# Kernel tuning notes

Measured on AMD Instinct MI355X. Metric: run time of the kernel, lower is better.

The kernel has to match this reference:

```python
import jax, jax.numpy as jnp
import numpy as np

DIM = 1024
HID = 2048
E = 4

def setup_inputs() -> dict:
    key = jax.random.key(0)
    ks = jax.random.split(key, 7)
    s = lambda fan_in: 1.0 / np.sqrt(fan_in)
    x = jax.random.normal(ks[0], (2, 2048, DIM), dtype=jnp.float32)
    W1 = jax.random.uniform(ks[1], (E, DIM, HID), jnp.float32, -s(DIM), s(DIM))
    b1 = jax.random.uniform(ks[2], (E, HID), jnp.float32, -s(DIM), s(DIM))
    W2 = jax.random.uniform(ks[3], (E, HID, DIM), jnp.float32, -s(HID), s(HID))
    b2 = jax.random.uniform(ks[4], (E, DIM), jnp.float32, -s(HID), s(HID))
    Wr = jax.random.uniform(ks[5], (DIM, E), jnp.float32, -s(DIM), s(DIM))
    br = jax.random.uniform(ks[6], (E,), jnp.float32, -s(DIM), s(DIM))
    return {"x": x, "W1": W1, "b1": b1, "W2": W2, "b2": b2, "Wr": Wr, "br": br}

def reference(x, W1, b1, W2, b2, Wr, br):
    # router softmax weights: [B,T,E]
    weights = jax.nn.softmax(x @ Wr + br, axis=-1)
    # all-expert MLP: hidden [B,T,E,H]
    h = jax.nn.gelu(jnp.einsum('btd,edh->bteh', x, W1) + b1, approximate=False)
    # expert outputs [B,T,E,D]
    y = jnp.einsum('bteh,ehd->bted', h, W2) + b2
    # softmax-weighted combine over experts
    return jnp.einsum('bte,bted->btd', weights, y)
```

## Files before the change

### kernel.cpp

```cpp
#include <hip/hip_runtime.h>
#include <hip/hip_bf16.h>
#include <math.h>

#define DIM 1024
#define HID 2048
#define NE  4
#define NT  4096
#define KW  (NE*HID)
#define KSPLIT 2
#define KCH (KW / KSPLIT)

typedef __attribute__((ext_vector_type(8))) short short8;
typedef __attribute__((ext_vector_type(4))) short short4v;
typedef __attribute__((ext_vector_type(4))) float floatx4;


__device__ __forceinline__ void async_cp16(const void* g, void* l) {
  __builtin_amdgcn_global_load_lds(
      (const __attribute__((address_space(1))) void*)g,
      (__attribute__((address_space(3))) void*)l, 16, 0, 0);
}

__device__ __forceinline__ short f2bf(float f) {
  union { float f; unsigned u; } x; x.f = f;
  unsigned r = x.u + 0x7fffu + ((x.u >> 16) & 1u);
  return (short)(r >> 16);
}

__device__ __forceinline__ float gelu_fast(float v) {
  float u = 1.595769122f * (v + 0.044715f * v * v * v);
  return v * __builtin_amdgcn_rcpf(1.0f + __expf(-u));
}

#define WBAR(N) do { \
    asm volatile("s_waitcnt vmcnt(" #N ")" ::: "memory"); \
    __builtin_amdgcn_s_barrier(); \
  } while (0)

__global__ void router_cvt(const float* __restrict__ x, const float* __restrict__ Wr,
                           const float* __restrict__ br, float* __restrict__ wgt,
                           short* __restrict__ xb) {
  const int wv = threadIdx.x >> 6, lane = threadIdx.x & 63;
  const int t = blockIdx.x * 4 + wv;
  const float* xr = x + (size_t)t * DIM;
  short* xo = xb + (size_t)t * DIM;
  float a0 = 0.f, a1 = 0.f, a2 = 0.f, a3 = 0.f;
  #pragma unroll
  for (int p = 0; p < 4; p++) {
    const int d = p * 256 + lane * 4;
    floatx4 v = *(const floatx4*)&xr[d];
    short4v o;
    #pragma unroll
    for (int j = 0; j < 4; j++) {
      o[j] = f2bf(v[j]);
      floatx4 wr = *(const floatx4*)&Wr[(d + j) * 4];
      a0 += v[j] * wr[0]; a1 += v[j] * wr[1];
      a2 += v[j] * wr[2]; a3 += v[j] * wr[3];
    }
    *(short4v*)&xo[d] = o;
  }
  #pragma unroll
  for (int off = 32; off; off >>= 1) {
    a0 += __shfl_down(a0, off);
    a1 += __shfl_down(a1, off);
    a2 += __shfl_down(a2, off);
    a3 += __shfl_down(a3, off);
  }
  a0 = __shfl(a0, 0); a1 = __shfl(a1, 0); a2 = __shfl(a2, 0); a3 = __shfl(a3, 0);
  float s0 = a0 + br[0], s1 = a1 + br[1], s2 = a2 + br[2], s3 = a3 + br[3];
  float m = fmaxf(fmaxf(s0, s1), fmaxf(s2, s3));
  float e0 = __expf(s0 - m), e1 = __expf(s1 - m), e2 = __expf(s2 - m), e3 = __expf(s3 - m);
  float inv = 1.f / (e0 + e1 + e2 + e3);
  float v = (lane == 0) ? e0 : (lane == 1) ? e1 : (lane == 2) ? e2 : e3;
  if (lane < 4) wgt[t * 4 + lane] = v * inv;
}

#define TP_PADR 136
__global__ void transpose_all(const float* __restrict__ W1, short* __restrict__ w1t,
                              const float* __restrict__ W2, short* __restrict__ w2t) {
  __shared__ __align__(16) short tile[32 * TP_PADR];
  const int b = blockIdx.x;
  const float* in; short* out; int R, C, xt, yt;
  if (b < 2048) {
    const int e = b >> 9, rem = b & 511;
    xt = rem & 63; yt = rem >> 6; R = DIM; C = HID;
    in = W1 + (size_t)e * DIM * HID; out = w1t + (size_t)e * DIM * HID;
  } else {
    const int rem = b - 2048;
    xt = rem & 31; yt = rem >> 5; R = KW; C = DIM;
    in = W2; out = w2t;
  }
  const int c0 = xt * 32, r0 = yt * 128;
  const int t = threadIdx.x;
  const int cin = (t & 7) * 4;
  const int rin = t >> 3;
  #pragma unroll
  for (int i = 0; i < 4; i++) {
    const int r = rin + i * 32;
    floatx4 v = *(const floatx4*)&in[(size_t)(r0 + r) * C + c0 + cin];
    #pragma unroll
    for (int j = 0; j < 4; j++)
      tile[(cin + j) * TP_PADR + r] = f2bf(v[j]);
  }
  __syncthreads();
  const int ct = t >> 3;
  #pragma unroll
  for (int i = 0; i < 2; i++) {
    const int rc = (t & 7) + 8 * i;
    short8 vv = *(const short8*)&tile[ct * TP_PADR + rc * 8];
    *(short8*)&out[(size_t)(c0 + ct) * R + r0 + rc * 8] = vv;
  }
}


__global__ __launch_bounds__(512, 2)
void gemm1_kernel(const short* __restrict__ xb, const short* __restrict__ w1t,
                  const float* __restrict__ b1, const float* __restrict__ wgt,
                  short* __restrict__ hw) {
  __shared__ __align__(16) short lds[65536];
  const int b = blockIdx.x;
  const int xcd = b & 7, slot = b >> 3;
  const int m0 = ((xcd & 3) * 4 + (slot & 3)) * 256;
  const int n0 = ((xcd >> 2) * 16 + (slot >> 2)) * 256;
  const int tid = threadIdx.x;
  const int lane = tid & 63, wv = tid >> 6;
  const int wm = (wv >> 2) * 128, wn = (wv & 3) * 64;
  const int quad = lane >> 4, lrow = lane & 15;

  const int srow = tid >> 3, su = (tid & 7) ^ (srow & 7);
  const int sm = 2 * srow + (su >> 2), skc = su & 3;
  const short* srcA0 = xb + (size_t)(m0 + sm) * DIM + skc * 8;
  const short* srcA1 = srcA0 + (size_t)128 * DIM;
  const short* srcB0 = w1t + (size_t)(n0 + sm) * DIM + skc * 8;
  const short* srcB1 = srcB0 + (size_t)128 * DIM;

  const int cswz = (quad | ((lrow & 1) << 2)) ^ (lrow >> 1);
  const int offA = ((wm >> 1) + (lrow >> 1)) * 64 + cswz * 8;
  const int offB = ((wn >> 1) + (lrow >> 1)) * 64 + cswz * 8;

  floatx4 acc[8][4];
  #pragma unroll
  for (int i = 0; i < 8; i++)
    #pragma unroll
    for (int j = 0; j < 4; j++) acc[i][j] = (floatx4)0.f;

#define G1_STAGE(sl, tk) do { \
    short* Ab = &lds[(sl) * 8192]; short* Bb = &lds[32768 + (sl) * 8192]; \
    async_cp16(srcA0 + (tk) * 32, Ab + tid * 8); \
    async_cp16(srcA1 + (tk) * 32, Ab + 4096 + tid * 8); \
    async_cp16(srcB0 + (tk) * 32, Bb + tid * 8); \
    async_cp16(srcB1 + (tk) * 32, Bb + 4096 + tid * 8); \
  } while (0)

#define G1_COMP(sl) do { \
    const short* Ab = &lds[(sl) * 8192]; const short* Bb = &lds[32768 + (sl) * 8192]; \
    short8 af[8], bfr[4]; \
    _Pragma("unroll") for (int i = 0; i < 8; i++) \
      af[i] = *(const short8*)&Ab[offA + i * 512]; \
    _Pragma("unroll") for (int j = 0; j < 4; j++) \
      bfr[j] = *(const short8*)&Bb[offB + j * 512]; \
    __builtin_amdgcn_s_setprio(1); \
    _Pragma("unroll") for (int i = 0; i < 8; i++) \
      _Pragma("unroll") for (int j = 0; j < 4; j++) \
        acc[i][j] = __builtin_amdgcn_mfma_f32_16x16x32_bf16(af[i], bfr[j], acc[i][j], 0, 0, 0); \
    __builtin_amdgcn_s_setprio(0); \
  } while (0)

  G1_STAGE(0, 0);
  G1_STAGE(1, 1);
  for (int t = 0; t < 28; t += 4) {
    G1_STAGE(2, t + 2); WBAR(8); G1_COMP(0);
    G1_STAGE(3, t + 3); WBAR(8); G1_COMP(1);
    G1_STAGE(0, t + 4); WBAR(8); G1_COMP(2);
    G1_STAGE(1, t + 5); WBAR(8); G1_COMP(3);
  }
  G1_STAGE(2, 30); WBAR(8); G1_COMP(0);
  G1_STAGE(3, 31); WBAR(8); G1_COMP(1);
  WBAR(4); G1_COMP(2);
  WBAR(0); G1_COMP(3);
#undef G1_STAGE
#undef G1_COMP

  const int e = n0 >> 11;
  #pragma unroll
  for (int i = 0; i < 8; i++) {
    const int rbase = m0 + wm + i * 16 + quad * 4;
    float w4[4];
    #pragma unroll
    for (int r = 0; r < 4; r++) w4[r] = wgt[(rbase + r) * NE + e];
    #pragma unroll
    for (int j = 0; j < 4; j++) {
      const int col = n0 + wn + j * 16 + lrow;
      const float b1v = b1[e * HID + (col & (HID - 1))];
      #pragma unroll
      for (int r = 0; r < 4; r++) {
        float v = acc[i][j][r] + b1v;
        hw[(size_t)(rbase + r) * KW + col] = f2bf(w4[r] * gelu_fast(v));
      }
    }
  }
}

__global__ __launch_bounds__(512, 2)
void gemm2_kernel(const short* __restrict__ hw, const short* __restrict__ w2t,
                  const float* __restrict__ b2, const float* __restrict__ wgt,
                  float* __restrict__ out, float* __restrict__ part) {
  __shared__ __align__(16) short lds[49152];
  const int b = blockIdx.x;
  const int xcd = b & 7, slot = b >> 3;
  const int kz = xcd >> 2;
  const int m0 = ((xcd & 3) * 4 + (slot & 3)) * 256;
  const int n0 = (slot >> 2) * 128;
  const int tid = threadIdx.x;
  const int lane = tid & 63, wv = tid >> 6;
  const int wm = (wv >> 1) * 64, wn = (wv & 1) * 64;
  const int quad = lane >> 4, lrow = lane & 15;

  const int srow = tid >> 3, su = (tid & 7) ^ (srow & 7);
  const int sm = 2 * srow + (su >> 2), skc = su & 3;
  const short* srcA0 = hw + (size_t)(m0 + sm) * KW + kz * KCH + skc * 8;
  const short* srcA1 = srcA0 + (size_t)128 * KW;
  const short* srcB0 = w2t + (size_t)(n0 + sm) * KW + kz * KCH + skc * 8;

  const int cswz = (quad | ((lrow & 1) << 2)) ^ (lrow >> 1);
  const int offA = ((wm >> 1) + (lrow >> 1)) * 64 + cswz * 8;
  const int offB = ((wn >> 1) + (lrow >> 1)) * 64 + cswz * 8;

  floatx4 acc[4][4];
  #pragma unroll
  for (int i = 0; i < 4; i++)
    #pragma unroll
    for (int j = 0; j < 4; j++) acc[i][j] = (floatx4)0.f;

#define G2_STAGE(sl, tk) do { \
    short* Ab = &lds[(sl) * 8192]; short* Bb = &lds[32768 + (sl) * 4096]; \
    async_cp16(srcA0 + (tk) * 32, Ab + tid * 8); \
    async_cp16(srcA1 + (tk) * 32, Ab + 4096 + tid * 8); \
    async_cp16(srcB0 + (tk) * 32, Bb + tid * 8); \
  } while (0)

#define G2_COMP(sl) do { \
    const short* Ab = &lds[(sl) * 8192]; const short* Bb = &lds[32768 + (sl) * 4096]; \
    short8 af[4], bfr[4]; \
    _Pragma("unroll") for (int i = 0; i < 4; i++) \
      af[i] = *(const short8*)&Ab[offA + i * 512]; \
    _Pragma("unroll") for (int j = 0; j < 4; j++) \
      bfr[j] = *(const short8*)&Bb[offB + j * 512]; \
    __builtin_amdgcn_s_setprio(1); \
    _Pragma("unroll") for (int i = 0; i < 4; i++) \
      _Pragma("unroll") for (int j = 0; j < 4; j++) \
        acc[i][j] = __builtin_amdgcn_mfma_f32_16x16x32_bf16(af[i], bfr[j], acc[i][j], 0, 0, 0); \
    __builtin_amdgcn_s_setprio(0); \
  } while (0)

  G2_STAGE(0, 0);
  G2_STAGE(1, 1);
  for (int t = 0; t < 124; t += 4) {
    G2_STAGE(2, t + 2); WBAR(6); G2_COMP(0);
    G2_STAGE(3, t + 3); WBAR(6); G2_COMP(1);
    G2_STAGE(0, t + 4); WBAR(6); G2_COMP(2);
    G2_STAGE(1, t + 5); WBAR(6); G2_COMP(3);
  }
  G2_STAGE(2, 126); WBAR(6); G2_COMP(0);
  G2_STAGE(3, 127); WBAR(6); G2_COMP(1);
  WBAR(3); G2_COMP(2);
  WBAR(0); G2_COMP(3);
#undef G2_STAGE
#undef G2_COMP

  if (kz == 0) {
    #pragma unroll
    for (int i = 0; i < 4; i++) {
      const int rbase = m0 + wm + i * 16 + quad * 4;
      floatx4 wr[4];
      #pragma unroll
      for (int r = 0; r < 4; r++) wr[r] = *(const floatx4*)&wgt[(rbase + r) * NE];
      #pragma unroll
      for (int j = 0; j < 4; j++) {
        const int col = n0 + wn + j * 16 + lrow;
        float b2v[4];
        #pragma unroll
        for (int eI = 0; eI < 4; eI++) b2v[eI] = b2[eI * DIM + col];
        #pragma unroll
        for (int r = 0; r < 4; r++) {
          float bias = wr[r][0] * b2v[0] + wr[r][1] * b2v[1] +
                       wr[r][2] * b2v[2] + wr[r][3] * b2v[3];
          out[(size_t)(rbase + r) * DIM + col] = acc[i][j][r] + bias;
        }
      }
    }
  } else {
    #pragma unroll
    for (int i = 0; i < 4; i++) {
      const int rbase = m0 + wm + i * 16 + quad * 4;
      #pragma unroll
      for (int j = 0; j < 4; j++) {
        const int col = n0 + wn + j * 16 + lrow;
        #pragma unroll
        for (int r = 0; r < 4; r++)
          part[(size_t)(rbase + r) * DIM + col] = acc[i][j][r];
      }
    }
  }
}

__global__ void reduce_out(float* __restrict__ out, const float* __restrict__ part) {
  int i = (blockIdx.x * 256 + threadIdx.x) * 4;
  floatx4 v = *(const floatx4*)&out[i];
  floatx4 a = *(const floatx4*)&part[i];
  v = v + a;
  *(floatx4*)&out[i] = v;
}


extern "C" void kernel_launch(void* const* d_in, const int* in_sizes, int n_in,
                              void* d_out, int out_size, void* d_ws, size_t ws_size,
                              hipStream_t stream) {
  const float* x  = (const float*)d_in[0];
  const float* W1 = (const float*)d_in[1];
  const float* b1 = (const float*)d_in[2];
  const float* W2 = (const float*)d_in[3];
  const float* b2 = (const float*)d_in[4];
  const float* Wr = (const float*)d_in[5];
  const float* br = (const float*)d_in[6];
  float* out = (float*)d_out;

  char* ws = (char*)d_ws;
  float* wgt = (float*)(ws);
  short* w2t = (short*)(ws + 65536);
  short* hw  = (short*)(ws + 65536 + 16777216);
  short* xb  = (short*)(ws + 65536 + 16777216 + 67108864);
  short* w1t = (short*)(ws + 65536 + 16777216 + 67108864 + 8388608);
  float* part= (float*)(ws + 65536 + 16777216 + 67108864);

  hipLaunchKernelGGL(router_cvt, dim3(NT / 4), dim3(256), 0, stream, x, Wr, br, wgt, xb);
  hipLaunchKernelGGL(transpose_all, dim3(2048 + 2048), dim3(256), 0, stream,
                     W1, w1t, W2, w2t);
  hipLaunchKernelGGL(gemm1_kernel, dim3(512), dim3(512), 0, stream,
                     xb, w1t, b1, wgt, hw);
  hipLaunchKernelGGL(gemm2_kernel, dim3(256), dim3(512), 0, stream,
                     hw, w2t, b2, wgt, out, part);
  hipLaunchKernelGGL(reduce_out, dim3(NT * DIM / 1024), dim3(256), 0, stream, out, part);
}
```

Measured before the change: 280.2 us.

## Split MFMA compute into two phases and interleave A/B async loads

Each per-slice compute step in both GEMM kernels is split into two halves that each load half of the A fragments. The B-tile async copies for the next stage are issued between the halves, so global loads are spread across the compute rather than issued in one burst. The vmcnt waits are adjusted to the new issue order. Fewer live fragment registers may ease register pressure and raise occupancy, at the cost of more interleaving complexity and possibly weaker latency hiding for the B loads.

```diff
diff --git a/kernel.cpp b/kernel.cpp
--- a/kernel.cpp
+++ b/kernel.cpp
@@ -32,10 +32,8 @@
   return v * __builtin_amdgcn_rcpf(1.0f + __expf(-u));
 }
 
-#define WBAR(N) do { \
-    asm volatile("s_waitcnt vmcnt(" #N ")" ::: "memory"); \
-    __builtin_amdgcn_s_barrier(); \
-  } while (0)
+#define VMW(n) asm volatile("s_waitcnt vmcnt(" #n ")" ::: "memory")
+#define BAR()  __builtin_amdgcn_s_barrier()
 
 __global__ void router_cvt(const float* __restrict__ x, const float* __restrict__ Wr,
                            const float* __restrict__ br, float* __restrict__ wgt,
@@ -144,42 +142,51 @@
     #pragma unroll
     for (int j = 0; j < 4; j++) acc[i][j] = (floatx4)0.f;
 
-#define G1_STAGE(sl, tk) do { \
-    short* Ab = &lds[(sl) * 8192]; short* Bb = &lds[32768 + (sl) * 8192]; \
+  short8 af[4], bfr[4];
+
+#define G1_SA(sl, tk) do { short* Ab = &lds[(sl) * 8192]; \
     async_cp16(srcA0 + (tk) * 32, Ab + tid * 8); \
-    async_cp16(srcA1 + (tk) * 32, Ab + 4096 + tid * 8); \
+    async_cp16(srcA1 + (tk) * 32, Ab + 4096 + tid * 8); } while (0)
+#define G1_SB(sl, tk) do { short* Bb = &lds[32768 + (sl) * 8192]; \
     async_cp16(srcB0 + (tk) * 32, Bb + tid * 8); \
-    async_cp16(srcB1 + (tk) * 32, Bb + 4096 + tid * 8); \
-  } while (0)
-
-#define G1_COMP(sl) do { \
+    async_cp16(srcB1 + (tk) * 32, Bb + 4096 + tid * 8); } while (0)
+
+#define G1_PH0(sl) do { \
     const short* Ab = &lds[(sl) * 8192]; const short* Bb = &lds[32768 + (sl) * 8192]; \
-    short8 af[8], bfr[4]; \
-    _Pragma("unroll") for (int i = 0; i < 8; i++) \
-      af[i] = *(const short8*)&Ab[offA + i * 512]; \
     _Pragma("unroll") for (int j = 0; j < 4; j++) \
       bfr[j] = *(const short8*)&Bb[offB + j * 512]; \
+    _Pragma("unroll") for (int i = 0; i < 4; i++) \
+      af[i] = *(const short8*)&Ab[offA + i * 512]; \
     __builtin_amdgcn_s_setprio(1); \
-    _Pragma("unroll") for (int i = 0; i < 8; i++) \
+    _Pragma("unroll") for (int i = 0; i < 4; i++) \
       _Pragma("unroll") for (int j = 0; j < 4; j++) \
         acc[i][j] = __builtin_amdgcn_mfma_f32_16x16x32_bf16(af[i], bfr[j], acc[i][j], 0, 0, 0); \
-    __builtin_amdgcn_s_setprio(0); \
-  } while (0)
-
-  G1_STAGE(0, 0);
-  G1_STAGE(1, 1);
+    __builtin_amdgcn_s_setprio(0); } while (0)
+#define G1_PH1(sl) do { \
+    const short* Ab = &lds[(sl) * 8192]; \
+    _Pragma("unroll") for (int i = 0; i < 4; i++) \
+      af[i] = *(const short8*)&Ab[offA + (4 + i) * 512]; \
+    __builtin_amdgcn_s_setprio(1); \
+    _Pragma("unroll") for (int i = 0; i < 4; i++) \
+      _Pragma("unroll") for (int j = 0; j < 4; j++) \
+        acc[4 + i][j] = __builtin_amdgcn_mfma_f32_16x16x32_bf16(af[i], bfr[j], acc[4 + i][j], 0, 0, 0); \
+    __builtin_amdgcn_s_setprio(0); } while (0)
+
+  G1_SA(0, 0); G1_SB(0, 0); G1_SA(1, 1); G1_SB(1, 1);
   for (int t = 0; t < 28; t += 4) {
-    G1_STAGE(2, t + 2); WBAR(8); G1_COMP(0);
-    G1_STAGE(3, t + 3); WBAR(8); G1_COMP(1);
-    G1_STAGE(0, t + 4); WBAR(8); G1_COMP(2);
-    G1_STAGE(1, t + 5); WBAR(8); G1_COMP(3);
-  }
-  G1_STAGE(2, 30); WBAR(8); G1_COMP(0);
-  G1_STAGE(3, 31); WBAR(8); G1_COMP(1);
-  WBAR(4); G1_COMP(2);
-  WBAR(0); G1_COMP(3);
-#undef G1_STAGE
-#undef G1_COMP
+    G1_SA(2, t + 2); VMW(6); BAR(); G1_PH0(0); G1_SB(2, t + 2); G1_PH1(0);
+    G1_SA(3, t + 3); VMW(6); BAR(); G1_PH0(1); G1_SB(3, t + 3); G1_PH1(1);
+    G1_SA(0, t + 4); VMW(6); BAR(); G1_PH0(2); G1_SB(0, t + 4); G1_PH1(2);
+    G1_SA(1, t + 5); VMW(6); BAR(); G1_PH0(3); G1_SB(1, t + 5); G1_PH1(3);
+  }
+  G1_SA(2, 30); VMW(6); BAR(); G1_PH0(0); G1_SB(2, 30); G1_PH1(0);
+  G1_SA(3, 31); VMW(6); BAR(); G1_PH0(1); G1_SB(3, 31); G1_PH1(1);
+  VMW(4); BAR(); G1_PH0(2); G1_PH1(2);
+  VMW(0); BAR(); G1_PH0(3); G1_PH1(3);
+#undef G1_SA
+#undef G1_SB
+#undef G1_PH0
+#undef G1_PH1
 
   const int e = n0 >> 11;
   #pragma unroll
@@ -232,41 +239,50 @@
     #pragma unroll
     for (int j = 0; j < 4; j++) acc[i][j] = (floatx4)0.f;
 
-#define G2_STAGE(sl, tk) do { \
-    short* Ab = &lds[(sl) * 8192]; short* Bb = &lds[32768 + (sl) * 4096]; \
+  short8 af[2], bfr[4];
+
+#define G2_SA(sl, tk) do { short* Ab = &lds[(sl) * 8192]; \
     async_cp16(srcA0 + (tk) * 32, Ab + tid * 8); \
-    async_cp16(srcA1 + (tk) * 32, Ab + 4096 + tid * 8); \
-    async_cp16(srcB0 + (tk) * 32, Bb + tid * 8); \
-  } while (0)
-
-#define G2_COMP(sl) do { \
+    async_cp16(srcA1 + (tk) * 32, Ab + 4096 + tid * 8); } while (0)
+#define G2_SB(sl, tk) do { short* Bb = &lds[32768 + (sl) * 4096]; \
+    async_cp16(srcB0 + (tk) * 32, Bb + tid * 8); } while (0)
+
+#define G2_PH0(sl) do { \
     const short* Ab = &lds[(sl) * 8192]; const short* Bb = &lds[32768 + (sl) * 4096]; \
-    short8 af[4], bfr[4]; \
-    _Pragma("unroll") for (int i = 0; i < 4; i++) \
-      af[i] = *(const short8*)&Ab[offA + i * 512]; \
     _Pragma("unroll") for (int j = 0; j < 4; j++) \
       bfr[j] = *(const short8*)&Bb[offB + j * 512]; \
+    _Pragma("unroll") for (int i = 0; i < 2; i++) \
+      af[i] = *(const short8*)&Ab[offA + i * 512]; \
     __builtin_amdgcn_s_setprio(1); \
-    _Pragma("unroll") for (int i = 0; i < 4; i++) \
+    _Pragma("unroll") for (int i = 0; i < 2; i++) \
       _Pragma("unroll") for (int j = 0; j < 4; j++) \
         acc[i][j] = __builtin_amdgcn_mfma_f32_16x16x32_bf16(af[i], bfr[j], acc[i][j], 0, 0, 0); \
-    __builtin_amdgcn_s_setprio(0); \
-  } while (0)
-
-  G2_STAGE(0, 0);
-  G2_STAGE(1, 1);
+    __builtin_amdgcn_s_setprio(0); } while (0)
+#define G2_PH1(sl) do { \
+    const short* Ab = &lds[(sl) * 8192]; \
+    _Pragma("unroll") for (int i = 0; i < 2; i++) \
+      af[i] = *(const short8*)&Ab[offA + (2 + i) * 512]; \
+    __builtin_amdgcn_s_setprio(1); \
+    _Pragma("unroll") for (int i = 0; i < 2; i++) \
+      _Pragma("unroll") for (int j = 0; j < 4; j++) \
+        acc[2 + i][j] = __builtin_amdgcn_mfma_f32_16x16x32_bf16(af[i], bfr[j], acc[2 + i][j], 0, 0, 0); \
+    __builtin_amdgcn_s_setprio(0); } while (0)
+
+  G2_SA(0, 0); G2_SB(0, 0); G2_SA(1, 1); G2_SB(1, 1);
   for (int t = 0; t < 124; t += 4) {
-    G2_STAGE(2, t + 2); WBAR(6); G2_COMP(0);
-    G2_STAGE(3, t + 3); WBAR(6); G2_COMP(1);
-    G2_STAGE(0, t + 4); WBAR(6); G2_COMP(2);
-    G2_STAGE(1, t + 5); WBAR(6); G2_COMP(3);
-  }
-  G2_STAGE(2, 126); WBAR(6); G2_COMP(0);
-  G2_STAGE(3, 127); WBAR(6); G2_COMP(1);
-  WBAR(3); G2_COMP(2);
-  WBAR(0); G2_COMP(3);
-#undef G2_STAGE
-#undef G2_COMP
+    G2_SA(2, t + 2); VMW(5); BAR(); G2_PH0(0); G2_SB(2, t + 2); G2_PH1(0);
+    G2_SA(3, t + 3); VMW(5); BAR(); G2_PH0(1); G2_SB(3, t + 3); G2_PH1(1);
+    G2_SA(0, t + 4); VMW(5); BAR(); G2_PH0(2); G2_SB(0, t + 4); G2_PH1(2);
+    G2_SA(1, t + 5); VMW(5); BAR(); G2_PH0(3); G2_SB(1, t + 5); G2_PH1(3);
+  }
+  G2_SA(2, 126); VMW(5); BAR(); G2_PH0(0); G2_SB(2, 126); G2_PH1(0);
+  G2_SA(3, 127); VMW(5); BAR(); G2_PH0(1); G2_SB(3, 127); G2_PH1(1);
+  VMW(3); BAR(); G2_PH0(2); G2_PH1(2);
+  VMW(0); BAR(); G2_PH0(3); G2_PH1(3);
+#undef G2_SA
+#undef G2_SB
+#undef G2_PH0
+#undef G2_PH1
 
   if (kz == 0) {
     #pragma unroll
```

Measured after the change: 278.9 us. No clear change (-0.5%).

## Merge prep kernels, overlap W2 transpose with gemm1, use double-buffered LDS

Applied to the files above, without the earlier changes.

Router/convert and the W1 transpose are merged into one prep kernel. The W2 transpose now runs as extra blocks inside the gemm1 launch, so it can overlap the GEMM and one launch is removed. Both GEMMs drop from a 4-stage to a 2-stage LDS pipeline with barriers on both sides of each compute step, halving shared memory per block. This may raise occupancy but exposes more load latency. The W2 transpose blocks in gemm1 may also compete with GEMM blocks for CUs.

```diff
diff --git a/kernel.cpp b/kernel.cpp
--- a/kernel.cpp
+++ b/kernel.cpp
@@ -32,64 +32,58 @@
   return v * __builtin_amdgcn_rcpf(1.0f + __expf(-u));
 }
 
-#define WBAR(N) do { \
-    asm volatile("s_waitcnt vmcnt(" #N ")" ::: "memory"); \
-    __builtin_amdgcn_s_barrier(); \
-  } while (0)
-
-__global__ void router_cvt(const float* __restrict__ x, const float* __restrict__ Wr,
-                           const float* __restrict__ br, float* __restrict__ wgt,
-                           short* __restrict__ xb) {
-  const int wv = threadIdx.x >> 6, lane = threadIdx.x & 63;
-  const int t = blockIdx.x * 4 + wv;
-  const float* xr = x + (size_t)t * DIM;
-  short* xo = xb + (size_t)t * DIM;
-  float a0 = 0.f, a1 = 0.f, a2 = 0.f, a3 = 0.f;
-  #pragma unroll
-  for (int p = 0; p < 4; p++) {
-    const int d = p * 256 + lane * 4;
-    floatx4 v = *(const floatx4*)&xr[d];
-    short4v o;
-    #pragma unroll
-    for (int j = 0; j < 4; j++) {
-      o[j] = f2bf(v[j]);
-      floatx4 wr = *(const floatx4*)&Wr[(d + j) * 4];
-      a0 += v[j] * wr[0]; a1 += v[j] * wr[1];
-      a2 += v[j] * wr[2]; a3 += v[j] * wr[3];
-    }
-    *(short4v*)&xo[d] = o;
-  }
-  #pragma unroll
-  for (int off = 32; off; off >>= 1) {
-    a0 += __shfl_down(a0, off);
-    a1 += __shfl_down(a1, off);
-    a2 += __shfl_down(a2, off);
-    a3 += __shfl_down(a3, off);
-  }
-  a0 = __shfl(a0, 0); a1 = __shfl(a1, 0); a2 = __shfl(a2, 0); a3 = __shfl(a3, 0);
-  float s0 = a0 + br[0], s1 = a1 + br[1], s2 = a2 + br[2], s3 = a3 + br[3];
-  float m = fmaxf(fmaxf(s0, s1), fmaxf(s2, s3));
-  float e0 = __expf(s0 - m), e1 = __expf(s1 - m), e2 = __expf(s2 - m), e3 = __expf(s3 - m);
-  float inv = 1.f / (e0 + e1 + e2 + e3);
-  float v = (lane == 0) ? e0 : (lane == 1) ? e1 : (lane == 2) ? e2 : e3;
-  if (lane < 4) wgt[t * 4 + lane] = v * inv;
-}
+#define VMW(n) asm volatile("s_waitcnt vmcnt(" #n ")" ::: "memory")
+#define BAR()  __builtin_amdgcn_s_barrier()
 
 #define TP_PADR 136
-__global__ void transpose_all(const float* __restrict__ W1, short* __restrict__ w1t,
-                              const float* __restrict__ W2, short* __restrict__ w2t) {
+
+__global__ void prep_kernel(const float* __restrict__ x, const float* __restrict__ Wr,
+                            const float* __restrict__ br, float* __restrict__ wgt,
+                            short* __restrict__ xb,
+                            const float* __restrict__ W1, short* __restrict__ w1t) {
   __shared__ __align__(16) short tile[32 * TP_PADR];
-  const int b = blockIdx.x;
-  const float* in; short* out; int R, C, xt, yt;
-  if (b < 2048) {
-    const int e = b >> 9, rem = b & 511;
-    xt = rem & 63; yt = rem >> 6; R = DIM; C = HID;
-    in = W1 + (size_t)e * DIM * HID; out = w1t + (size_t)e * DIM * HID;
-  } else {
-    const int rem = b - 2048;
-    xt = rem & 31; yt = rem >> 5; R = KW; C = DIM;
-    in = W2; out = w2t;
-  }
+  if (blockIdx.x < 1024) {
+    const int wv = threadIdx.x >> 6, lane = threadIdx.x & 63;
+    const int t = blockIdx.x * 4 + wv;
+    const float* xr = x + (size_t)t * DIM;
+    short* xo = xb + (size_t)t * DIM;
+    float a0 = 0.f, a1 = 0.f, a2 = 0.f, a3 = 0.f;
+    #pragma unroll
+    for (int p = 0; p < 4; p++) {
+      const int d = p * 256 + lane * 4;
+      floatx4 v = *(const floatx4*)&xr[d];
+      short4v o;
+      #pragma unroll
+      for (int j = 0; j < 4; j++) {
+        o[j] = f2bf(v[j]);
+        floatx4 wr = *(const floatx4*)&Wr[(d + j) * 4];
+        a0 += v[j] * wr[0]; a1 += v[j] * wr[1];
+        a2 += v[j] * wr[2]; a3 += v[j] * wr[3];
+      }
+      *(short4v*)&xo[d] = o;
+    }
+    #pragma unroll
+    for (int off = 32; off; off >>= 1) {
+      a0 += __shfl_down(a0, off);
+      a1 += __shfl_down(a1, off);
+      a2 += __shfl_down(a2, off);
+      a3 += __shfl_down(a3, off);
+    }
+    a0 = __shfl(a0, 0); a1 = __shfl(a1, 0); a2 = __shfl(a2, 0); a3 = __shfl(a3, 0);
+    float s0 = a0 + br[0], s1 = a1 + br[1], s2 = a2 + br[2], s3 = a3 + br[3];
+    float m = fmaxf(fmaxf(s0, s1), fmaxf(s2, s3));
+    float e0 = __expf(s0 - m), e1 = __expf(s1 - m), e2 = __expf(s2 - m), e3 = __expf(s3 - m);
+    float inv = 1.f / (e0 + e1 + e2 + e3);
+    float v = (lane == 0) ? e0 : (lane == 1) ? e1 : (lane == 2) ? e2 : e3;
+    if (lane < 4) wgt[t * 4 + lane] = v * inv;
+    return;
+  }
+  const int b = blockIdx.x - 1024;
+  const int e = b >> 9, rem = b & 511;
+  const int xt = rem & 63, yt = rem >> 6;
+  const int R = DIM, C = HID;
+  const float* in = W1 + (size_t)e * DIM * HID;
+  short* out = w1t + (size_t)e * DIM * HID;
   const int c0 = xt * 32, r0 = yt * 128;
   const int t = threadIdx.x;
   const int cin = (t & 7) * 4;
@@ -116,13 +110,43 @@
 __global__ __launch_bounds__(512, 2)
 void gemm1_kernel(const short* __restrict__ xb, const short* __restrict__ w1t,
                   const float* __restrict__ b1, const float* __restrict__ wgt,
-                  short* __restrict__ hw) {
-  __shared__ __align__(16) short lds[65536];
+                  short* __restrict__ hw,
+                  const float* __restrict__ W2, short* __restrict__ w2t) {
+  __shared__ __align__(16) short lds[32768];
   const int b = blockIdx.x;
+  const int tid = threadIdx.x;
+
+  if (b >= 512) {
+    const int sub = tid >> 8;
+    const int tt = tid & 255;
+    const int tileIdx = (b - 512) * 2 + sub;
+    const int xt = tileIdx & 31, yt = tileIdx >> 5;
+    const int c0 = xt * 32, r0 = yt * 128;
+    short* tile = lds + sub * (32 * TP_PADR);
+    const int cin = (tt & 7) * 4;
+    const int rin = tt >> 3;
+    #pragma unroll
+    for (int i = 0; i < 4; i++) {
+      const int r = rin + i * 32;
+      floatx4 v = *(const floatx4*)&W2[(size_t)(r0 + r) * DIM + c0 + cin];
+      #pragma unroll
+      for (int j = 0; j < 4; j++)
+        tile[(cin + j) * TP_PADR + r] = f2bf(v[j]);
+    }
+    __syncthreads();
+    const int ct = tt >> 3;
+    #pragma unroll
+    for (int i = 0; i < 2; i++) {
+      const int rc = (tt & 7) + 8 * i;
+      short8 vv = *(const short8*)&tile[ct * TP_PADR + rc * 8];
+      *(short8*)&w2t[(size_t)(c0 + ct) * KW + r0 + rc * 8] = vv;
+    }
+    return;
+  }
+
   const int xcd = b & 7, slot = b >> 3;
   const int m0 = ((xcd & 3) * 4 + (slot & 3)) * 256;
   const int n0 = ((xcd >> 2) * 16 + (slot >> 2)) * 256;
-  const int tid = threadIdx.x;
   const int lane = tid & 63, wv = tid >> 6;
   const int wm = (wv >> 2) * 128, wn = (wv & 3) * 64;
   const int quad = lane >> 4, lrow = lane & 15;
@@ -145,15 +169,15 @@
     for (int j = 0; j < 4; j++) acc[i][j] = (floatx4)0.f;
 
 #define G1_STAGE(sl, tk) do { \
-    short* Ab = &lds[(sl) * 8192]; short* Bb = &lds[32768 + (sl) * 8192]; \
-    async_cp16(srcA0 + (tk) * 32, Ab + tid * 8); \
-    async_cp16(srcA1 + (tk) * 32, Ab + 4096 + tid * 8); \
-    async_cp16(srcB0 + (tk) * 32, Bb + tid * 8); \
-    async_cp16(srcB1 + (tk) * 32, Bb + 4096 + tid * 8); \
+    short* Ab = &lds[(sl) * 8192]; short* Bb = &lds[16384 + (sl) * 8192]; \
+    async_cp16(srcA0 + (size_t)(tk) * 32, Ab + tid * 8); \
+    async_cp16(srcA1 + (size_t)(tk) * 32, Ab + 4096 + tid * 8); \
+    async_cp16(srcB0 + (size_t)(tk) * 32, Bb + tid * 8); \
+    async_cp16(srcB1 + (size_t)(tk) * 32, Bb + 4096 + tid * 8); \
   } while (0)
 
 #define G1_COMP(sl) do { \
-    const short* Ab = &lds[(sl) * 8192]; const short* Bb = &lds[32768 + (sl) * 8192]; \
+    const short* Ab = &lds[(sl) * 8192]; const short* Bb = &lds[16384 + (sl) * 8192]; \
     short8 af[8], bfr[4]; \
     _Pragma("unroll") for (int i = 0; i < 8; i++) \
       af[i] = *(const short8*)&Ab[offA + i * 512]; \
@@ -163,21 +187,15 @@
     _Pragma("unroll") for (int i = 0; i < 8; i++) \
       _Pragma("unroll") for (int j = 0; j < 4; j++) \
         acc[i][j] = __builtin_amdgcn_mfma_f32_16x16x32_bf16(af[i], bfr[j], acc[i][j], 0, 0, 0); \
-    __builtin_amdgcn_s_setprio(0); \
-  } while (0)
+    __builtin_amdgcn_s_setprio(0); } while (0)
 
   G1_STAGE(0, 0);
-  G1_STAGE(1, 1);
-  for (int t = 0; t < 28; t += 4) {
-    G1_STAGE(2, t + 2); WBAR(8); G1_COMP(0);
-    G1_STAGE(3, t + 3); WBAR(8); G1_COMP(1);
-    G1_STAGE(0, t + 4); WBAR(8); G1_COMP(2);
-    G1_STAGE(1, t + 5); WBAR(8); G1_COMP(3);
-  }
-  G1_STAGE(2, 30); WBAR(8); G1_COMP(0);
-  G1_STAGE(3, 31); WBAR(8); G1_COMP(1);
-  WBAR(4); G1_COMP(2);
-  WBAR(0); G1_COMP(3);
+  for (int t = 0; t < 30; t += 2) {
+    G1_STAGE(1, t + 1); VMW(4); BAR(); G1_COMP(0); BAR();
+    G1_STAGE(0, t + 2); VMW(4); BAR(); G1_COMP(1); BAR();
+  }
+  G1_STAGE(1, 31); VMW(4); BAR(); G1_COMP(0); BAR();
+  VMW(0); BAR(); G1_COMP(1);
 #undef G1_STAGE
 #undef G1_COMP
 
@@ -205,7 +223,7 @@
 void gemm2_kernel(const short* __restrict__ hw, const short* __restrict__ w2t,
                   const float* __restrict__ b2, const float* __restrict__ wgt,
                   float* __restrict__ out, float* __restrict__ part) {
-  __shared__ __align__(16) short lds[49152];
+  __shared__ __align__(16) short lds[24576];
   const int b = blockIdx.x;
   const int xcd = b & 7, slot = b >> 3;
   const int kz = xcd >> 2;
@@ -233,14 +251,14 @@
     for (int j = 0; j < 4; j++) acc[i][j] = (floatx4)0.f;
 
 #define G2_STAGE(sl, tk) do { \
-    short* Ab = &lds[(sl) * 8192]; short* Bb = &lds[32768 + (sl) * 4096]; \
-    async_cp16(srcA0 + (tk) * 32, Ab + tid * 8); \
-    async_cp16(srcA1 + (tk) * 32, Ab + 4096 + tid * 8); \
-    async_cp16(srcB0 + (tk) * 32, Bb + tid * 8); \
+    short* Ab = &lds[(sl) * 8192]; short* Bb = &lds[16384 + (sl) * 4096]; \
+    async_cp16(srcA0 + (size_t)(tk) * 32, Ab + tid * 8); \
+    async_cp16(srcA1 + (size_t)(tk) * 32, Ab + 4096 + tid * 8); \
+    async_cp16(srcB0 + (size_t)(tk) * 32, Bb + tid * 8); \
   } while (0)
 
 #define G2_COMP(sl) do { \
-    const short* Ab = &lds[(sl) * 8192]; const short* Bb = &lds[32768 + (sl) * 4096]; \
+    const short* Ab = &lds[(sl) * 8192]; const short* Bb = &lds[16384 + (sl) * 4096]; \
     short8 af[4], bfr[4]; \
     _Pragma("unroll") for (int i = 0; i < 4; i++) \
       af[i] = *(const short8*)&Ab[offA + i * 512]; \
@@ -250,21 +268,15 @@
     _Pragma("unroll") for (int i = 0; i < 4; i++) \
       _Pragma("unroll") for (int j = 0; j < 4; j++) \
         acc[i][j] = __builtin_amdgcn_mfma_f32_16x16x32_bf16(af[i], bfr[j], acc[i][j], 0, 0, 0); \
-    __builtin_amdgcn_s_setprio(0); \
-  } while (0)
+    __builtin_amdgcn_s_setprio(0); } while (0)
 
   G2_STAGE(0, 0);
-  G2_STAGE(1, 1);
-  for (int t = 0; t < 124; t += 4) {
-    G2_STAGE(2, t + 2); WBAR(6); G2_COMP(0);
-    G2_STAGE(3, t + 3); WBAR(6); G2_COMP(1);
-    G2_STAGE(0, t + 4); WBAR(6); G2_COMP(2);
-    G2_STAGE(1, t + 5); WBAR(6); G2_COMP(3);
-  }
-  G2_STAGE(2, 126); WBAR(6); G2_COMP(0);
-  G2_STAGE(3, 127); WBAR(6); G2_COMP(1);
-  WBAR(3); G2_COMP(2);
-  WBAR(0); G2_COMP(3);
+  for (int t = 0; t < 126; t += 2) {
+    G2_STAGE(1, t + 1); VMW(3); BAR(); G2_COMP(0); BAR();
+    G2_STAGE(0, t + 2); VMW(3); BAR(); G2_COMP(1); BAR();
+  }
+  G2_STAGE(1, 127); VMW(3); BAR(); G2_COMP(0); BAR();
+  VMW(0); BAR(); G2_COMP(1);
 #undef G2_STAGE
 #undef G2_COMP
 
@@ -333,11 +345,10 @@
   short* w1t = (short*)(ws + 65536 + 16777216 + 67108864 + 8388608);
   float* part= (float*)(ws + 65536 + 16777216 + 67108864);
 
-  hipLaunchKernelGGL(router_cvt, dim3(NT / 4), dim3(256), 0, stream, x, Wr, br, wgt, xb);
-  hipLaunchKernelGGL(transpose_all, dim3(2048 + 2048), dim3(256), 0, stream,
-                     W1, w1t, W2, w2t);
-  hipLaunchKernelGGL(gemm1_kernel, dim3(512), dim3(512), 0, stream,
-                     xb, w1t, b1, wgt, hw);
+  hipLaunchKernelGGL(prep_kernel, dim3(1024 + 2048), dim3(256), 0, stream,
+                     x, Wr, br, wgt, xb, W1, w1t);
+  hipLaunchKernelGGL(gemm1_kernel, dim3(512 + 1024), dim3(512), 0, stream,
+                     xb, w1t, b1, wgt, hw, W2, w2t);
   hipLaunchKernelGGL(gemm2_kernel, dim3(256), dim3(512), 0, stream,
                      hw, w2t, b2, wgt, out, part);
   hipLaunchKernelGGL(reduce_out, dim3(NT * DIM / 1024), dim3(256), 0, stream, out, part);
```

New measurement: 282.3 us. No clear change (+0.8%).
